# Kernel optimization log

Measured on AMD Instinct MI355X. Metric: run time of the kernel, lower is better.

The kernel has to match this reference:

```python
import jax, jax.numpy as jnp
import numpy as np

LATENT_DIM = 512


def setup_inputs() -> dict:
    key = jax.random.key(0)
    k1, k2, k3, k4 = jax.random.split(key, 4)
    B, C, H, W = 8, 256, 1, 65536  # W is a multiple of LATENT_DIM -> adaptive pool == binned mean
    x = jax.random.normal(k1, (B, C, H, W), dtype=jnp.float32)
    conv_w = jax.random.normal(k2, (1, C), dtype=jnp.float32) * (1.0 / np.sqrt(C))
    conv_b = jax.random.normal(k3, (1,), dtype=jnp.float32)
    eps = jax.random.normal(k4, (LATENT_DIM,), dtype=jnp.float32)  # reparam noise (vectorized rsample)
    return {"x": x, "conv_w": conv_w, "conv_b": conv_b, "eps": eps}


def reference(x, conv_w, conv_b, eps):
    B, C, H, W = x.shape
    L = eps.shape[0]
    # 1x1 Conv2d(channels -> 1): pure channel contraction
    o = jnp.einsum('bchw,oc->bohw', x, conv_w) + conv_b[None, :, None, None]  # [B,1,H,W]
    # AdaptiveAvgPool1d(L) over last dim; W % L == 0 so each bin averages W//L elems
    o_b = o.reshape(B, 1, H, L, W // L)
    mean = o_b.mean(axis=-1)               # [B,1,H,L]
    mean_sq = (o_b * o_b).mean(axis=-1)    # [B,1,H,L]
    std = jnp.sqrt(mean_sq - mean * mean)  # [B,1,H,L]
    # original loops over batch 0's concatenated [mean, std] vector and draws
    # z_i = Normal(mean_i, std_i).rsample(); vectorized reparameterization:
    m0 = mean[0, 0, 0]  # [L]
    s0 = std[0, 0, 0]   # [L]
    latent = m0 + s0 * eps
    return latent[None, :]  # [1, L]
```

## Files before the change

### kernel.cpp

```cpp
#include <hip/hip_runtime.h>
#include <hip/hip_bf16.h>

#define XW   65536
#define XC   256
#define XL   512
#define BIN  128

__global__ __launch_bounds__(256) void statspool_kernel(
    const float* __restrict__ x,
    const float* __restrict__ cw,
    const float* __restrict__ cb,
    const float* __restrict__ eps,
    float* __restrict__ out)
{
    const int l  = blockIdx.x;
    const int t  = threadIdx.x;
    const int wi = t & 63;
    const int cg = t >> 6;

    const int w0 = l * BIN + (wi << 1);
    const float* xp = x + (size_t)cg * 64 * XW + w0;

    float a0 = 0.f, a1 = 0.f;
    #pragma unroll 8
    for (int c = 0; c < 64; ++c) {
        const float wc = cw[(cg << 6) + c];
        const float2 v = *(const float2*)(xp + (size_t)c * XW);
        a0 = fmaf(wc, v.x, a0);
        a1 = fmaf(wc, v.y, a1);
    }

    __shared__ float part0[4][64];
    __shared__ float part1[4][64];
    part0[cg][wi] = a0;
    part1[cg][wi] = a1;
    __syncthreads();

    if (t < 64) {
        const float b  = cb[0];
        const float o0 = part0[0][wi] + part0[1][wi] + part0[2][wi] + part0[3][wi] + b;
        const float o1 = part1[0][wi] + part1[1][wi] + part1[2][wi] + part1[3][wi] + b;
        float s  = o0 + o1;
        float sq = fmaf(o0, o0, o1 * o1);

        #pragma unroll
        for (int off = 32; off; off >>= 1) {
            s  += __shfl_down(s,  off);
            sq += __shfl_down(sq, off);
        }

        if (wi == 0) {
            const float inv  = 1.0f / (float)BIN;
            const float mean = s * inv;
            const float msq  = sq * inv;
            const float var  = fmaxf(msq - mean * mean, 0.0f);
            out[l] = fmaf(sqrtf(var), eps[l], mean);
        }
    }
}

extern "C" void kernel_launch(void* const* d_in, const int* in_sizes, int n_in,
                              void* d_out, int out_size, void* d_ws, size_t ws_size,
                              hipStream_t stream) {
    const float* x   = (const float*)d_in[0];
    const float* cw  = (const float*)d_in[1];
    const float* cb  = (const float*)d_in[2];
    const float* eps = (const float*)d_in[3];
    float* out = (float*)d_out;

    statspool_kernel<<<dim3(XL), dim3(256), 0, stream>>>(x, cw, cb, eps, out);
}
```

Baseline: 15.92 us.

## Split channel reduction across 32 groups with float4 loads in 1024-thread blocks

Each block now uses 1024 threads: 32 channel groups of 8 channels each, with every thread loading float4 chunks of the bin instead of float2 across 64 channels. Partial sums go to a larger shared buffer and are reduced by 128 threads before the stats wave. The goal is more memory-level parallelism per block and wider loads on a latency-bound read of batch 0's channels. In exchange it adds a second shared-memory reduction stage and a barrier, and uses larger blocks.

```diff
diff --git a/kernel.cpp b/kernel.cpp
--- a/kernel.cpp
+++ b/kernel.cpp
@@ -6,7 +6,7 @@
 #define XL   512
 #define BIN  128
 
-__global__ __launch_bounds__(256) void statspool_kernel(
+__global__ __launch_bounds__(1024) void statspool_kernel(
     const float* __restrict__ x,
     const float* __restrict__ cw,
     const float* __restrict__ cb,
@@ -15,41 +15,49 @@
 {
     const int l  = blockIdx.x;
     const int t  = threadIdx.x;
-    const int wi = t & 63;
-    const int cg = t >> 6;
+    const int wi = t & 31;
+    const int cg = t >> 5;
 
-    const int w0 = l * BIN + (wi << 1);
-    const float* xp = x + (size_t)cg * 64 * XW + w0;
+    const float4 wA = *(const float4*)(cw + (cg << 3));
+    const float4 wB = *(const float4*)(cw + (cg << 3) + 4);
+    const float wgt[8] = {wA.x, wA.y, wA.z, wA.w, wB.x, wB.y, wB.z, wB.w};
 
-    float a0 = 0.f, a1 = 0.f;
-    #pragma unroll 8
-    for (int c = 0; c < 64; ++c) {
-        const float wc = cw[(cg << 6) + c];
-        const float2 v = *(const float2*)(xp + (size_t)c * XW);
-        a0 = fmaf(wc, v.x, a0);
-        a1 = fmaf(wc, v.y, a1);
+    const float* xp = x + (size_t)(cg << 3) * XW + l * BIN + (wi << 2);
+
+    float4 acc = make_float4(0.f, 0.f, 0.f, 0.f);
+    #pragma unroll
+    for (int c = 0; c < 8; ++c) {
+        const float4 v = *(const float4*)(xp + (size_t)c * XW);
+        acc.x = fmaf(wgt[c], v.x, acc.x);
+        acc.y = fmaf(wgt[c], v.y, acc.y);
+        acc.z = fmaf(wgt[c], v.z, acc.z);
+        acc.w = fmaf(wgt[c], v.w, acc.w);
     }
 
-    __shared__ float part0[4][64];
-    __shared__ float part1[4][64];
-    part0[cg][wi] = a0;
-    part1[cg][wi] = a1;
+    __shared__ float part[32 * BIN];
+    __shared__ float ob[BIN];
+    *(float4*)(part + (cg << 7) + (wi << 2)) = acc;
+    __syncthreads();
+
+    if (t < BIN) {
+        float s = 0.f;
+        #pragma unroll
+        for (int g = 0; g < 32; ++g) s += part[(g << 7) + t];
+        ob[t] = s + cb[0];
+    }
     __syncthreads();
 
     if (t < 64) {
-        const float b  = cb[0];
-        const float o0 = part0[0][wi] + part0[1][wi] + part0[2][wi] + part0[3][wi] + b;
-        const float o1 = part1[0][wi] + part1[1][wi] + part1[2][wi] + part1[3][wi] + b;
+        const float o0 = ob[t];
+        const float o1 = ob[t + 64];
         float s  = o0 + o1;
         float sq = fmaf(o0, o0, o1 * o1);
-
         #pragma unroll
         for (int off = 32; off; off >>= 1) {
             s  += __shfl_down(s,  off);
             sq += __shfl_down(sq, off);
         }
-
-        if (wi == 0) {
+        if (t == 0) {
             const float inv  = 1.0f / (float)BIN;
             const float mean = s * inv;
             const float msq  = sq * inv;
@@ -68,5 +76,5 @@
     const float* eps = (const float*)d_in[3];
     float* out = (float*)d_out;
 
-    statspool_kernel<<<dim3(XL), dim3(256), 0, stream>>>(x, cw, cb, eps, out);
+    statspool_kernel<<<dim3(XL), dim3(1024), 0, stream>>>(x, cw, cb, eps, out);
 }
```

New measurement: 16.29 us. 1.02x slower.

## Split conv-pool into channel-group partial pass and separate reduction pass

Applied to the files above, without the earlier changes.

Replaces the single fused kernel with two kernels: the first computes per-channel-group partial dot products over wide float4 spans into a workspace, the second sums groups per bin and computes mean/std and the reparameterized output. Intent is to raise memory-level parallelism and load width on the 64 MB read. It adds a workspace round trip and an extra launch, with a fallback to the old kernel if workspace is small.

```diff
diff --git a/kernel.cpp b/kernel.cpp
--- a/kernel.cpp
+++ b/kernel.cpp
@@ -6,11 +6,80 @@
 #define XL   512
 #define BIN  128
 
-__global__ __launch_bounds__(256) void statspool_kernel(
+#define NG    16
+#define NSPAN 32
+#define SPANW (XW / NSPAN)
+
+__global__ __launch_bounds__(512) void statspool_phaseA(
     const float* __restrict__ x,
     const float* __restrict__ cw,
+    float* __restrict__ part)
+{
+    const int b  = blockIdx.x;
+    const int g  = b & (NG - 1);
+    const int ws = b >> 4;
+    const int t  = threadIdx.x;
+
+    const int w0 = ws * SPANW + (t << 2);
+    const float* xp = x + (size_t)(g * 16) * XW + w0;
+
+    float4 acc = make_float4(0.f, 0.f, 0.f, 0.f);
+    #pragma unroll
+    for (int cs = 0; cs < 16; ++cs) {
+        const float wc = cw[g * 16 + cs];
+        const float4 v = *(const float4*)(xp + (size_t)cs * XW);
+        acc.x = fmaf(wc, v.x, acc.x);
+        acc.y = fmaf(wc, v.y, acc.y);
+        acc.z = fmaf(wc, v.z, acc.z);
+        acc.w = fmaf(wc, v.w, acc.w);
+    }
+    *(float4*)(part + (size_t)g * XW + w0) = acc;
+}
+
+__global__ __launch_bounds__(256) void statspool_phaseB(
+    const float* __restrict__ part,
     const float* __restrict__ cb,
     const float* __restrict__ eps,
+    float* __restrict__ out)
+{
+    const int l = blockIdx.x;
+    const int t = threadIdx.x;
+    const int j  = t & 127;
+    const int gh = t >> 7;
+
+    const float* pp = part + (size_t)gh * 8 * XW + l * BIN + j;
+    float s = 0.f;
+    #pragma unroll
+    for (int g = 0; g < 8; ++g) s += pp[(size_t)g * XW];
+
+    __shared__ float sm[2][BIN];
+    sm[gh][j] = s;
+    __syncthreads();
+
+    if (t < 64) {
+        const float bsv = cb[0];
+        const float o0 = sm[0][t]      + sm[1][t]      + bsv;
+        const float o1 = sm[0][t + 64] + sm[1][t + 64] + bsv;
+        float su = o0 + o1;
+        float sq = fmaf(o0, o0, o1 * o1);
+        #pragma unroll
+        for (int off = 32; off; off >>= 1) {
+            su += __shfl_down(su, off);
+            sq += __shfl_down(sq, off);
+        }
+        if (t == 0) {
+            const float inv  = 1.0f / (float)BIN;
+            const float mean = su * inv;
+            const float msq  = sq * inv;
+            const float var  = fmaxf(msq - mean * mean, 0.0f);
+            out[l] = fmaf(sqrtf(var), eps[l], mean);
+        }
+    }
+}
+
+__global__ __launch_bounds__(256) void statspool_fallback(
+    const float* __restrict__ x, const float* __restrict__ cw,
+    const float* __restrict__ cb, const float* __restrict__ eps,
     float* __restrict__ out)
 {
     const int l  = blockIdx.x;
@@ -29,26 +98,22 @@
         a0 = fmaf(wc, v.x, a0);
         a1 = fmaf(wc, v.y, a1);
     }
-
     __shared__ float part0[4][64];
     __shared__ float part1[4][64];
     part0[cg][wi] = a0;
     part1[cg][wi] = a1;
     __syncthreads();
-
     if (t < 64) {
         const float b  = cb[0];
         const float o0 = part0[0][wi] + part0[1][wi] + part0[2][wi] + part0[3][wi] + b;
         const float o1 = part1[0][wi] + part1[1][wi] + part1[2][wi] + part1[3][wi] + b;
         float s  = o0 + o1;
         float sq = fmaf(o0, o0, o1 * o1);
-
         #pragma unroll
         for (int off = 32; off; off >>= 1) {
             s  += __shfl_down(s,  off);
             sq += __shfl_down(sq, off);
         }
-
         if (wi == 0) {
             const float inv  = 1.0f / (float)BIN;
             const float mean = s * inv;
@@ -68,5 +133,12 @@
     const float* eps = (const float*)d_in[3];
     float* out = (float*)d_out;
 
-    statspool_kernel<<<dim3(XL), dim3(256), 0, stream>>>(x, cw, cb, eps, out);
+    const size_t need = (size_t)NG * XW * sizeof(float);
+    if (ws_size >= need) {
+        float* part = (float*)d_ws;
+        statspool_phaseA<<<dim3(NG * NSPAN), dim3(512), 0, stream>>>(x, cw, part);
+        statspool_phaseB<<<dim3(XL), dim3(256), 0, stream>>>(part, cb, eps, out);
+    } else {
+        statspool_fallback<<<dim3(XL), dim3(256), 0, stream>>>(x, cw, cb, eps, out);
+    }
 }
```

Measured after the change: 19.85 us. +24.7%, slower.
